# Kernel tuning notes

Hardware: AMD Instinct MI355X
Metric: run time of the kernel (lower is better)

## Reference

```python
import jax, jax.numpy as jnp
import numpy as np

N = 50000      # nodes
E = 800000     # edges
F_IN = 500     # input features
H1 = 300       # lin output
H2 = 100       # conv1 output
C = 16         # num classes


def setup_inputs() -> dict:
    key = jax.random.key(0)
    ks = jax.random.split(key, 8)
    x = jax.random.normal(ks[0], (N, F_IN), dtype=jnp.float32)
    edge_index = jax.random.randint(ks[1], (2, E), 0, N, dtype=jnp.int64)
    s = 0.05
    lin_W = jax.random.normal(ks[2], (F_IN, H1), dtype=jnp.float32) * s
    lin_b = jnp.zeros((H1,), dtype=jnp.float32)
    W1 = jax.random.normal(ks[3], (H1, H2), dtype=jnp.float32) * s
    b1 = jnp.zeros((H2,), dtype=jnp.float32)
    W2 = jax.random.normal(ks[4], (H2, C), dtype=jnp.float32) * s
    b2 = jnp.zeros((C,), dtype=jnp.float32)
    return {"x": x, "lin_W": lin_W, "lin_b": lin_b, "W1": W1, "b1": b1,
            "W2": W2, "b2": b2, "edge_index": edge_index}


def gcn_layer(x, W, b, src, dst):
    # project first (PyG GCNConv), then normalized gather-scatter aggregation
    h = x @ W                                   # [N, d_out]
    loops = jnp.arange(N, dtype=src.dtype)      # add self-loops
    s = jnp.concatenate([src, loops])           # [E+N]
    d = jnp.concatenate([dst, loops])
    deg = jax.ops.segment_sum(jnp.ones_like(d, dtype=h.dtype), d, num_segments=N)
    dinv = jax.lax.rsqrt(jnp.maximum(deg, 1.0))  # deg >= 1 due to self-loops
    norm = dinv[s] * dinv[d]                     # [E+N]
    out = jax.ops.segment_sum(h[s] * norm[:, None], d, num_segments=N)
    return out + b


def reference(x, lin_W, lin_b, W1, b1, W2, b2, edge_index):
    src, dst = edge_index[0], edge_index[1]
    h = jax.nn.relu(x @ lin_W + lin_b)          # Linear(500->300) + relu
    h = jax.nn.relu(gcn_layer(h, W1, b1, src, dst))  # GCNConv(300->100) + relu
    # dropout is identity at inference (training=False)
    h = gcn_layer(h, W2, b2, src, dst)          # GCNConv(100->16)
    return jax.nn.log_softmax(h, axis=1)
```

## Files before the change

kernel.cpp:

```cpp
#include <hip/hip_runtime.h>
#include <hip/hip_bf16.h>

#define NN 50000
#define EE 800000
#define FIN 500
#define H1D 300
#define H2D 100
#define CC 16
#define GNB 196
#define PREP_N1 196608
#define PREP_N2 40960
#define PREP_BLOCKS 928

__device__ __forceinline__ float ldf(const void* p, size_t i, int isbf16) {
    return isbf16 ? __bfloat162float(((const __hip_bfloat16*)p)[i])
                  : ((const float*)p)[i];
}
__device__ __forceinline__ int ld_src(const int* ei, int e, int is64) {
    return is64 ? ei[2 * (size_t)e] : ei[e];
}
__device__ __forceinline__ int ld_dst(const int* ei, int e, int is64) {
    return is64 ? ei[2 * ((size_t)EE + e)] : ei[(size_t)EE + e];
}

__device__ __forceinline__ void split2(float f, unsigned short& h, unsigned short& l) {
    __bf16 hb = (__bf16)f;
    float fh = (float)hb;
    __bf16 lb = (__bf16)(f - fh);
    h = __builtin_bit_cast(unsigned short, hb);
    l = __builtin_bit_cast(unsigned short, lb);
}

__device__ __forceinline__ float2 bf2f2(unsigned int v) {
    float lo = __builtin_bit_cast(float, v << 16);
    float hi = __builtin_bit_cast(float, v & 0xffff0000u);
    return make_float2(lo, hi);
}

typedef __bf16 bf16x8 __attribute__((ext_vector_type(8)));
typedef float f32x4 __attribute__((ext_vector_type(4)));

__device__ __forceinline__ void prep_body(int idx, const float* linW, const float* W1,
                                          unsigned short* Bt1, unsigned short* Bt2) {
    if (idx < PREP_N1) {
        int n = idx >> 9, k = idx & 511;
        float v = (n < H1D && k < FIN) ? linW[(size_t)k * H1D + n] : 0.0f;
        unsigned short h, l;
        split2(v, h, l);
        Bt1[(size_t)n * 1024 + k] = h;
        Bt1[(size_t)n * 1024 + 512 + k] = l;
    } else if (idx < PREP_N1 + PREP_N2) {
        idx -= PREP_N1;
        int n = idx / 320, k = idx - n * 320;
        float v = (n < H2D && k < H1D) ? W1[(size_t)k * H2D + n] : 0.0f;
        unsigned short h, l;
        split2(v, h, l);
        Bt2[(size_t)n * 640 + k] = h;
        Bt2[(size_t)n * 640 + 320 + k] = l;
    }
}

__global__ __launch_bounds__(256) void k_init(const unsigned short* __restrict__ xw,
                                              const unsigned int* __restrict__ ew,
                                              int* __restrict__ flags,
                                              int* __restrict__ cnt,
                                              int* __restrict__ total,
                                              const float* __restrict__ linW,
                                              const float* __restrict__ W1,
                                              unsigned short* __restrict__ Bt1,
                                              unsigned short* __restrict__ Bt2) {
    int b = blockIdx.x;
    if (b == 0) {
        __shared__ int c_sane, c_zero;
        if (threadIdx.x == 0) { c_sane = 0; c_zero = 0; }
        __syncthreads();
        int t = threadIdx.x;
        int sane = 0, zer = 0;
        for (int j = 0; j < 4; j++) {
            unsigned short w = xw[t * 4 + j];
            int ex = (w >> 7) & 0xFF;
            if (w == 0 || (ex >= 100 && ex <= 150)) sane++;
            if (ew[2 * (t * 4 + j) + 1] == 0u) zer++;
        }
        atomicAdd(&c_sane, sane);
        atomicAdd(&c_zero, zer);
        __syncthreads();
        if (threadIdx.x == 0) {
            flags[0] = (c_sane > 820) ? 1 : 0;
            flags[1] = (c_zero > 512) ? 1 : 0;
            total[0] = 0;
        }
    } else if (b <= GNB) {
        int i = (b - 1) * 256 + threadIdx.x;
        if (i < NN) cnt[i] = 0;
    } else {
        prep_body((b - GNB - 1) * 256 + threadIdx.x, linW, W1, Bt1, Bt2);
    }
}

__global__ __launch_bounds__(256) void k_prep_both(const float* __restrict__ linW,
                                                   const float* __restrict__ W1,
                                                   unsigned short* __restrict__ Bt1,
                                                   unsigned short* __restrict__ Bt2,
                                                   const int* __restrict__ flags) {
    if (flags[0]) return;
    prep_body(blockIdx.x * 256 + threadIdx.x, linW, W1, Bt1, Bt2);
}

__global__ void k_hist(const int* __restrict__ ei, int* __restrict__ cnt,
                       const int* __restrict__ flags) {
    int e = blockIdx.x * blockDim.x + threadIdx.x;
    int is64 = flags[1];
    if (e < EE) {
        int d = ld_dst(ei, e, is64);
        if ((unsigned)d < NN) atomicAdd(&cnt[d], 1);
    }
}

__global__ __launch_bounds__(256) void k_scan_mb(int* __restrict__ cnt,
                                                 int* __restrict__ row_ptr,
                                                 float* __restrict__ dinv,
                                                 int* __restrict__ total) {
    int t = threadIdx.x;
    int i = blockIdx.x * 256 + t;
    int c = (i < NN) ? cnt[i] : 0;
    __shared__ int s[256];
    s[t] = c;
    __syncthreads();
    for (int off = 1; off < 256; off <<= 1) {
        int v = (t >= off) ? s[t - off] : 0;
        __syncthreads();
        s[t] += v;
        __syncthreads();
    }
    int incl = s[t];
    __shared__ int base;
    if (t == 255) base = atomicAdd(total, s[255]);
    __syncthreads();
    if (i < NN) {
        row_ptr[i] = base + incl - c;
        dinv[i] = rsqrtf((float)c + 1.0f);
        cnt[i] = 0;
    }
}

__global__ void k_scatter(const int* __restrict__ ei, const int* __restrict__ row_ptr,
                          int* __restrict__ fill, int* __restrict__ csr_src,
                          const int* __restrict__ flags) {
    int e = blockIdx.x * blockDim.x + threadIdx.x;
    int is64 = flags[1];
    if (e < EE) {
        int s = ld_src(ei, e, is64);
        int d = ld_dst(ei, e, is64);
        if ((unsigned)d < NN) {
            int pos = row_ptr[d] + atomicAdd(&fill[d], 1);
            csr_src[pos] = s;
        }
    }
}

template <bool A_DYN, bool RELU, bool SCALE, bool OUTBF>
__global__ __launch_bounds__(256) void k_gemm(const void* __restrict__ A,
                                              const void* __restrict__ B,
                                              const void* __restrict__ bias,
                                              const float* __restrict__ dinv,
                                              void* __restrict__ C,
                                              int M, int K, int Nn,
                                              const int* __restrict__ flags) {
    if (!flags[0]) return;
    __shared__ float As[16][68];
    __shared__ float Bs[16][68];
    const int bf = flags[0];
    const int tid = threadIdx.x;
    const int m0 = blockIdx.x * 64, n0 = blockIdx.y * 64;
    const int tx = tid & 15;
    const int ty = tid >> 4;
    float acc[4][4] = {};

    for (int kc = 0; kc < K; kc += 16) {
#pragma unroll
        for (int j = 0; j < 4; j++) {
            int idx = tid + j * 256;
            int kk = idx & 15, mm = idx >> 4;
            int gm = m0 + mm, gk = kc + kk;
            float v = 0.0f;
            if (gm < M && gk < K) {
                size_t o = (size_t)gm * K + gk;
                v = A_DYN ? ldf(A, o, bf) : ((const float*)A)[o];
            }
            As[kk][mm] = v;
        }
#pragma unroll
        for (int j = 0; j < 4; j++) {
            int idx = tid + j * 256;
            int nn = idx & 63, kk = idx >> 6;
            int gk = kc + kk, gn = n0 + nn;
            Bs[kk][nn] = (gk < K && gn < Nn) ? ldf(B, (size_t)gk * Nn + gn, bf) : 0.0f;
        }
        __syncthreads();
#pragma unroll
        for (int kk = 0; kk < 16; kk++) {
            float4 a4 = *(const float4*)&As[kk][ty * 4];
            float4 b4 = *(const float4*)&Bs[kk][tx * 4];
            float av[4] = {a4.x, a4.y, a4.z, a4.w};
            float bv[4] = {b4.x, b4.y, b4.z, b4.w};
#pragma unroll
            for (int i = 0; i < 4; i++)
#pragma unroll
                for (int j = 0; j < 4; j++) acc[i][j] += av[i] * bv[j];
        }
        __syncthreads();
    }

#pragma unroll
    for (int i = 0; i < 4; i++) {
        int m = m0 + ty * 4 + i;
        if (m >= M) continue;
        float sc = SCALE ? dinv[m] : 1.0f;
#pragma unroll
        for (int j = 0; j < 4; j++) {
            int n = n0 + tx * 4 + j;
            if (n >= Nn) continue;
            float v = acc[i][j];
            if (bias) v += ldf(bias, n, bf);
            if (SCALE) v *= sc;
            if (RELU) v = fmaxf(v, 0.0f);
            if (OUTBF) ((__hip_bfloat16*)C)[(size_t)m * Nn + n] = __float2bfloat16(v);
            else       ((float*)C)[(size_t)m * Nn + n] = v;
        }
    }
}

template <int BM, int WN, bool RELU, bool SCALE, bool HAS_BIAS, bool OUTBF>
__global__ __launch_bounds__(256) void k_gemm_mfma_split(const float* __restrict__ A,
                                                         const unsigned short* __restrict__ Bt,
                                                         const float* __restrict__ bias,
                                                         const float* __restrict__ dinv,
                                                         void* __restrict__ C,
                                                         int M, int K, int Kp, int Nn, int NnS,
                                                         const int* __restrict__ flags) {
    if (flags[0]) return;
    constexpr int WM = 4 / WN;
    constexpr int FM = BM / WM / 16;
    constexpr int FN = 128 / WN / 16;
    constexpr int NA = BM / 32;
    __shared__ unsigned short As_hi[BM * 32], As_lo[BM * 32];
    __shared__ unsigned short Bs_hi[4096], Bs_lo[4096];
    const int tid = threadIdx.x;
    const int nbx = gridDim.x;
    const int Wt = nbx * gridDim.y;
    const int li = blockIdx.x + nbx * blockIdx.y;
    const int q8 = Wt >> 3, r8 = Wt & 7;
    const int xk = li & 7, xj = li >> 3;
    const int wid = (xk < r8 ? xk * (q8 + 1) : r8 * (q8 + 1) + (xk - r8) * q8) + xj;
    const int n0 = (wid % nbx) * 128;
    const int m0 = (wid / nbx) * BM;
    const int w = tid >> 6, l = tid & 63;
    const int wm = (w / WN) * (BM / WM);
    const int wn = (w % WN) * (128 / WN);
    const int lr = l & 15, ls = l >> 4;
    f32x4 acc[FM][FN] = {};

    float4 stA[NA];
    uint4  stB0, stB1, stB2, stB3;

#define LOAD_TILE(kc_)                                                              \
    {                                                                               \
        int kc = (kc_);                                                             \
        _Pragma("unroll")                                                           \
        for (int j = 0; j < NA; j++) {                                              \
            int c = tid + j * 256;                                                  \
            int r = c >> 3, q = c & 7;                                              \
            int gm = m0 + r, gk = kc + q * 4;                                       \
            stA[j] = (gm < M && gk < K) ? *(const float4*)(A + (size_t)gm * K + gk) \
                                        : make_float4(0.f, 0.f, 0.f, 0.f);          \
        }                                                                           \
        {                                                                           \
            int c, r, q, gn;                                                        \
            c = tid;       r = c >> 2; q = c & 3; gn = n0 + r;                      \
            stB0 = *(const uint4*)(Bt + (size_t)gn * (2 * Kp) + kc + q * 8);        \
            c = tid + 256; r = c >> 2; q = c & 3; gn = n0 + r;                      \
            stB1 = *(const uint4*)(Bt + (size_t)gn * (2 * Kp) + kc + q * 8);        \
            c = tid;       r = c >> 2; q = c & 3; gn = n0 + r;                      \
            stB2 = *(const uint4*)(Bt + (size_t)gn * (2 * Kp) + Kp + kc + q * 8);   \
            c = tid + 256; r = c >> 2; q = c & 3; gn = n0 + r;                      \
            stB3 = *(const uint4*)(Bt + (size_t)gn * (2 * Kp) + Kp + kc + q * 8);   \
        }                                                                           \
    }

#define WRITE_TILE()                                                                \
    {                                                                               \
        _Pragma("unroll")                                                           \
        for (int j = 0; j < NA; j++) {                                              \
            int c = tid + j * 256;                                                  \
            int r = c >> 3, q = c & 7;                                              \
            unsigned short h0,h1,h2,h3,l0,l1,l2,l3;                                 \
            split2(stA[j].x, h0, l0); split2(stA[j].y, h1, l1);                     \
            split2(stA[j].z, h2, l2); split2(stA[j].w, h3, l3);                     \
            int waddr = r * 64 + (((q >> 1) ^ ((r >> 1) & 3)) << 4) + ((q & 1) << 3); \
            *(ushort4*)((char*)As_hi + waddr) = make_ushort4(h0, h1, h2, h3);       \
            *(ushort4*)((char*)As_lo + waddr) = make_ushort4(l0, l1, l2, l3);       \
        }                                                                           \
        {                                                                           \
            int c, r, q, waddr;                                                     \
            c = tid;       r = c >> 2; q = c & 3; waddr = r * 64 + ((q ^ ((r >> 1) & 3)) << 4); \
            *(uint4*)((char*)Bs_hi + waddr) = stB0;                                 \
            c = tid + 256; r = c >> 2; q = c & 3; waddr = r * 64 + ((q ^ ((r >> 1) & 3)) << 4); \
            *(uint4*)((char*)Bs_hi + waddr) = stB1;                                 \
            c = tid;       r = c >> 2; q = c & 3; waddr = r * 64 + ((q ^ ((r >> 1) & 3)) << 4); \
            *(uint4*)((char*)Bs_lo + waddr) = stB2;                                 \
            c = tid + 256; r = c >> 2; q = c & 3; waddr = r * 64 + ((q ^ ((r >> 1) & 3)) << 4); \
            *(uint4*)((char*)Bs_lo + waddr) = stB3;                                 \
        }                                                                           \
    }

    const int nsteps = (K + 31) / 32;
    LOAD_TILE(0);
    for (int kt = 0; kt < nsteps; kt++) {
        WRITE_TILE();
        __syncthreads();
        if (kt + 1 < nsteps) LOAD_TILE((kt + 1) * 32);
        bf16x8 ah[FM], al[FM], bh[FN], bl[FN];
#pragma unroll
        for (int fm = 0; fm < FM; fm++) {
            int rr = wm + fm * 16 + lr;
            int addr = rr * 64 + ((ls ^ ((rr >> 1) & 3)) << 4);
            ah[fm] = *(const bf16x8*)((const char*)As_hi + addr);
            al[fm] = *(const bf16x8*)((const char*)As_lo + addr);
        }
#pragma unroll
        for (int fn = 0; fn < FN; fn++) {
            int cc2 = wn + fn * 16 + lr;
            int addr = cc2 * 64 + ((ls ^ ((cc2 >> 1) & 3)) << 4);
            bh[fn] = *(const bf16x8*)((const char*)Bs_hi + addr);
            bl[fn] = *(const bf16x8*)((const char*)Bs_lo + addr);
        }
#pragma unroll
        for (int fm = 0; fm < FM; fm++)
#pragma unroll
            for (int fn = 0; fn < FN; fn++) {
                acc[fm][fn] = __builtin_amdgcn_mfma_f32_16x16x32_bf16(ah[fm], bh[fn], acc[fm][fn], 0, 0, 0);
                acc[fm][fn] = __builtin_amdgcn_mfma_f32_16x16x32_bf16(ah[fm], bl[fn], acc[fm][fn], 0, 0, 0);
                acc[fm][fn] = __builtin_amdgcn_mfma_f32_16x16x32_bf16(al[fm], bh[fn], acc[fm][fn], 0, 0, 0);
            }
        __syncthreads();
    }
#undef LOAD_TILE
#undef WRITE_TILE

#pragma unroll
    for (int fm = 0; fm < FM; fm++) {
#pragma unroll
        for (int j = 0; j < 4; j++) {
            int m = m0 + wm + fm * 16 + ls * 4 + j;
            if (m >= M) continue;
            float sc = SCALE ? dinv[m] : 1.0f;
#pragma unroll
            for (int fn = 0; fn < FN; fn++) {
                int n = n0 + wn + fn * 16 + lr;
                if (OUTBF) {
                    if (n >= NnS) continue;
                    float v = 0.0f;
                    if (n < Nn) {
                        v = acc[fm][fn][j];
                        if (HAS_BIAS) v += bias[n];
                        if (SCALE) v *= sc;
                        if (RELU) v = fmaxf(v, 0.0f);
                    }
                    ((__hip_bfloat16*)C)[(size_t)m * NnS + n] = __float2bfloat16(v);
                } else {
                    if (n >= Nn) continue;
                    float v = acc[fm][fn][j];
                    if (HAS_BIAS) v += bias[n];
                    if (SCALE) v *= sc;
                    if (RELU) v = fmaxf(v, 0.0f);
                    ((float*)C)[(size_t)m * Nn + n] = v;
                }
            }
        }
    }
}

__global__ __launch_bounds__(256) void k_gemm2_bf16a(const unsigned short* __restrict__ A,
                                                     const unsigned short* __restrict__ Bt,
                                                     const float* __restrict__ dinv,
                                                     unsigned short* __restrict__ C,
                                                     int M, const int* __restrict__ flags) {
    if (flags[0]) return;
    constexpr int Kp = 320;
    __shared__ unsigned short As[64 * 32];
    __shared__ unsigned short Bs_hi[4096], Bs_lo[4096];
    const int tid = threadIdx.x;
    const int Wt = gridDim.x;
    const int li = blockIdx.x;
    const int q8 = Wt >> 3, r8 = Wt & 7;
    const int xk = li & 7, xj = li >> 3;
    const int wid = (xk < r8 ? xk * (q8 + 1) : r8 * (q8 + 1) + (xk - r8) * q8) + xj;
    const int m0 = wid * 64;
    const int w = tid >> 6, l = tid & 63;
    const int wn = w * 32;
    const int lr = l & 15, ls = l >> 4;
    f32x4 acc[4][2] = {};

    uint4 stA, stB0, stB1, stB2, stB3;

#define LOAD_T2(kc_)                                                                \
    {                                                                               \
        int kc = (kc_);                                                             \
        {                                                                           \
            int r = tid >> 2, q = tid & 3;                                          \
            int gm = m0 + r;                                                        \
            stA = (gm < M) ? *(const uint4*)(A + (size_t)gm * Kp + kc + q * 8)      \
                           : make_uint4(0u, 0u, 0u, 0u);                            \
        }                                                                           \
        {                                                                           \
            int c, r, q, gn;                                                        \
            c = tid;       r = c >> 2; q = c & 3; gn = r;                           \
            stB0 = *(const uint4*)(Bt + (size_t)gn * (2 * Kp) + kc + q * 8);        \
            c = tid + 256; r = c >> 2; q = c & 3; gn = r;                           \
            stB1 = *(const uint4*)(Bt + (size_t)gn * (2 * Kp) + kc + q * 8);        \
            c = tid;       r = c >> 2; q = c & 3; gn = r;                           \
            stB2 = *(const uint4*)(Bt + (size_t)gn * (2 * Kp) + Kp + kc + q * 8);   \
            c = tid + 256; r = c >> 2; q = c & 3; gn = r;                           \
            stB3 = *(const uint4*)(Bt + (size_t)gn * (2 * Kp) + Kp + kc + q * 8);   \
        }                                                                           \
    }

#define WRITE_T2()                                                                  \
    {                                                                               \
        {                                                                           \
            int r = tid >> 2, q = tid & 3;                                          \
            int waddr = r * 64 + ((q ^ ((r >> 1) & 3)) << 4);                       \
            *(uint4*)((char*)As + waddr) = stA;                                     \
        }                                                                           \
        {                                                                           \
            int c, r, q, waddr;                                                     \
            c = tid;       r = c >> 2; q = c & 3; waddr = r * 64 + ((q ^ ((r >> 1) & 3)) << 4); \
            *(uint4*)((char*)Bs_hi + waddr) = stB0;                                 \
            c = tid + 256; r = c >> 2; q = c & 3; waddr = r * 64 + ((q ^ ((r >> 1) & 3)) << 4); \
            *(uint4*)((char*)Bs_hi + waddr) = stB1;                                 \
            c = tid;       r = c >> 2; q = c & 3; waddr = r * 64 + ((q ^ ((r >> 1) & 3)) << 4); \
            *(uint4*)((char*)Bs_lo + waddr) = stB2;                                 \
            c = tid + 256; r = c >> 2; q = c & 3; waddr = r * 64 + ((q ^ ((r >> 1) & 3)) << 4); \
            *(uint4*)((char*)Bs_lo + waddr) = stB3;                                 \
        }                                                                           \
    }

    const int nsteps = Kp / 32;
    LOAD_T2(0);
    for (int kt = 0; kt < nsteps; kt++) {
        WRITE_T2();
        __syncthreads();
        if (kt + 1 < nsteps) LOAD_T2((kt + 1) * 32);
        bf16x8 ah[4], bh[2], bl[2];
#pragma unroll
        for (int fm = 0; fm < 4; fm++) {
            int rr = fm * 16 + lr;
            int addr = rr * 64 + ((ls ^ ((rr >> 1) & 3)) << 4);
            ah[fm] = *(const bf16x8*)((const char*)As + addr);
        }
#pragma unroll
        for (int fn = 0; fn < 2; fn++) {
            int cc2 = wn + fn * 16 + lr;
            int addr = cc2 * 64 + ((ls ^ ((cc2 >> 1) & 3)) << 4);
            bh[fn] = *(const bf16x8*)((const char*)Bs_hi + addr);
            bl[fn] = *(const bf16x8*)((const char*)Bs_lo + addr);
        }
#pragma unroll
        for (int fm = 0; fm < 4; fm++)
#pragma unroll
            for (int fn = 0; fn < 2; fn++) {
                acc[fm][fn] = __builtin_amdgcn_mfma_f32_16x16x32_bf16(ah[fm], bh[fn], acc[fm][fn], 0, 0, 0);
                acc[fm][fn] = __builtin_amdgcn_mfma_f32_16x16x32_bf16(ah[fm], bl[fn], acc[fm][fn], 0, 0, 0);
            }
        __syncthreads();
    }
#undef LOAD_T2
#undef WRITE_T2

#pragma unroll
    for (int fm = 0; fm < 4; fm++) {
#pragma unroll
        for (int j = 0; j < 4; j++) {
            int m = m0 + fm * 16 + ls * 4 + j;
            if (m >= M) continue;
            float sc = dinv[m];
#pragma unroll
            for (int fn = 0; fn < 2; fn++) {
                int n = wn + fn * 16 + lr;
                if (n >= H2D) continue;
                ((__hip_bfloat16*)C)[(size_t)m * H2D + n] = __float2bfloat16(acc[fm][fn][j] * sc);
            }
        }
    }
}

__global__ __launch_bounds__(256) void k_agg1_fused(const unsigned short* __restrict__ h1p_bf,
                                                    const int* __restrict__ row_ptr,
                                                    const int* __restrict__ deg,
                                                    const int* __restrict__ csr_src,
                                                    const float* __restrict__ dinv,
                                                    const void* __restrict__ b1,
                                                    const void* __restrict__ W2,
                                                    float* __restrict__ h2p,
                                                    const int* __restrict__ flags) {
    __shared__ float W2s[16][105];
    __shared__ float b1s[H2D];
    __shared__ float Hrow[4][H2D];
    const int bf = flags[0];
    const int tid = threadIdx.x;
    for (int i = tid; i < H2D * CC; i += 256) {
        int k = i >> 4, n = i & 15;
        W2s[n][k] = ldf(W2, i, bf);
    }
    for (int i = tid; i < H2D; i += 256) b1s[i] = ldf(b1, i, bf);
    __syncthreads();

    const int w = tid >> 6, lane = tid & 63;
    const int q = lane >> 4, n16 = lane & 15;
    const unsigned int* rows = (const unsigned int*)h1p_bf;
    for (int node = blockIdx.x * 4 + w; node < NN; node += gridDim.x * 4) {
        float di = dinv[node];
        if (lane < 50) {
            float2 s = bf2f2(rows[(size_t)node * 50 + lane]);
            float a0x = s.x, a0y = s.y;
            float a1x = 0.f, a1y = 0.f, a2x = 0.f, a2y = 0.f, a3x = 0.f, a3y = 0.f;
            int lo = row_ptr[node], hi = lo + deg[node];
            int e = lo;
            for (; e + 3 < hi; e += 4) {
                int s0 = csr_src[e], s1 = csr_src[e + 1], s2 = csr_src[e + 2], s3 = csr_src[e + 3];
                float2 v0 = bf2f2(rows[(size_t)s0 * 50 + lane]);
                float2 v1 = bf2f2(rows[(size_t)s1 * 50 + lane]);
                float2 v2 = bf2f2(rows[(size_t)s2 * 50 + lane]);
                float2 v3 = bf2f2(rows[(size_t)s3 * 50 + lane]);
                a0x += v0.x; a0y += v0.y;
                a1x += v1.x; a1y += v1.y;
                a2x += v2.x; a2y += v2.y;
                a3x += v3.x; a3y += v3.y;
            }
            for (; e < hi; e++) {
                float2 v = bf2f2(rows[(size_t)csr_src[e] * 50 + lane]);
                a0x += v.x; a0y += v.y;
            }
            float sx = (a0x + a1x) + (a2x + a3x);
            float sy = (a0y + a1y) + (a2y + a3y);
            int f = lane * 2;
            Hrow[w][f]     = fmaxf(sx * di + b1s[f], 0.0f);
            Hrow[w][f + 1] = fmaxf(sy * di + b1s[f + 1], 0.0f);
        }
        __builtin_amdgcn_sched_barrier(0);
        float acc2 = 0.0f;
#pragma unroll
        for (int j = 0; j < 25; j++) {
            int k = q * 25 + j;
            acc2 += Hrow[w][k] * W2s[n16][k];
        }
        acc2 += __shfl_xor(acc2, 16);
        acc2 += __shfl_xor(acc2, 32);
        if (lane < 16) h2p[(size_t)node * CC + n16] = acc2 * di;
        __builtin_amdgcn_sched_barrier(0);
    }
}

__global__ __launch_bounds__(256) void k_agg2(const float* __restrict__ h2p,
                                              const int* __restrict__ row_ptr,
                                              const int* __restrict__ deg,
                                              const int* __restrict__ csr_src,
                                              const float* __restrict__ dinv,
                                              const void* __restrict__ b2,
                                              void* __restrict__ out,
                                              const int* __restrict__ flags) {
    int tid = threadIdx.x;
    int n = tid & 15;
    int g = tid >> 4;
    int node = blockIdx.x * 16 + g;
    if (node >= NN) return;
    const int bf = flags[0];
    float a0 = h2p[(size_t)node * CC + n];
    float a1 = 0.f, a2 = 0.f, a3 = 0.f;
    int lo = row_ptr[node], hi = lo + deg[node];
    int e = lo;
    for (; e + 3 < hi; e += 4) {
        int s0 = csr_src[e], s1 = csr_src[e + 1], s2 = csr_src[e + 2], s3 = csr_src[e + 3];
        a0 += h2p[(size_t)s0 * CC + n];
        a1 += h2p[(size_t)s1 * CC + n];
        a2 += h2p[(size_t)s2 * CC + n];
        a3 += h2p[(size_t)s3 * CC + n];
    }
    for (; e < hi; e++) a0 += h2p[(size_t)csr_src[e] * CC + n];
    float acc = (a0 + a1) + (a2 + a3);
    float logit = acc * dinv[node] + ldf(b2, n, bf);
    float m = logit;
#pragma unroll
    for (int off = 1; off < 16; off <<= 1) m = fmaxf(m, __shfl_xor(m, off, 16));
    float ex = __expf(logit - m);
    float ssum = ex;
#pragma unroll
    for (int off = 1; off < 16; off <<= 1) ssum += __shfl_xor(ssum, off, 16);
    float r = logit - m - __logf(ssum);
    size_t oidx = (size_t)node * CC + n;
    if (bf) ((__hip_bfloat16*)out)[oidx] = __float2bfloat16(r);
    else    ((float*)out)[oidx] = r;
}

extern "C" void kernel_launch(void* const* d_in, const int* in_sizes, int n_in,
                              void* d_out, int out_size, void* d_ws, size_t ws_size,
                              hipStream_t stream) {
    const void* x     = d_in[0];
    const void* lin_W = d_in[1];
    const void* lin_b = d_in[2];
    const void* W1    = d_in[3];
    const void* b1    = d_in[4];
    const void* W2    = d_in[5];
    const void* b2    = d_in[6];
    const int*  ei    = (const int*)d_in[7];

    char* ws = (char*)d_ws;
    size_t off = 0;
    auto alloc = [&](size_t bytes) {
        off = (off + 255) & ~(size_t)255;
        void* p = ws + off;
        off += bytes;
        return p;
    };
    int*   flags   = (int*)alloc(2 * 4);
    int*   total   = (int*)alloc(4);
    int*   cnt     = (int*)alloc((size_t)NN * 4);
    int*   row_ptr = (int*)alloc((size_t)NN * 4);
    int*   csr_src = (int*)alloc((size_t)EE * 4);
    float* dinv    = (float*)alloc((size_t)NN * 4);
    char*  H1      = (char*)alloc((size_t)NN * H1D * 4);
    unsigned short* H1p = (unsigned short*)alloc((size_t)NN * H2D * 2);
    float* h2p     = (float*)alloc((size_t)NN * CC * 4);
    unsigned short* Bt1 = (unsigned short*)alloc((size_t)384 * 1024 * 2);
    unsigned short* Bt2 = (unsigned short*)alloc((size_t)128 * 640 * 2);

    const int gE = (EE + 255) / 256;

    const bool surely_fp32 = (in_sizes != nullptr) && (in_sizes[0] >= 90000000);

    k_init<<<surely_fp32 ? (GNB + 1 + PREP_BLOCKS) : (GNB + 1), 256, 0, stream>>>(
        (const unsigned short*)x, (const unsigned int*)ei, flags, cnt, total,
        (const float*)lin_W, (const float*)W1, Bt1, Bt2);
    if (!surely_fp32)
        k_prep_both<<<PREP_BLOCKS, 256, 0, stream>>>(
            (const float*)lin_W, (const float*)W1, Bt1, Bt2, flags);

    k_hist<<<gE, 256, 0, stream>>>(ei, cnt, flags);
    k_scan_mb<<<GNB, 256, 0, stream>>>(cnt, row_ptr, dinv, total);
    k_scatter<<<gE, 256, 0, stream>>>(ei, row_ptr, cnt, csr_src, flags);

    {
        const int moff[5] = {0, 12544, 25088, 37632, 50000};
        for (int qi = 0; qi < 4; qi++) {
            int Mq = moff[qi + 1] - moff[qi];
            int nb = (Mq + 63) / 64;
            k_gemm_mfma_split<64, 4, true, false, true, true>
                <<<dim3(3, nb), 256, 0, stream>>>(
                    (const float*)x + (size_t)moff[qi] * FIN, Bt1, (const float*)lin_b,
                    nullptr, (unsigned short*)H1 + (size_t)moff[qi] * 320,
                    Mq, FIN, 512, H1D, 320, flags);
        }
    }
    if (!surely_fp32) {
        dim3 grid((NN + 63) / 64, (H1D + 63) / 64);
        k_gemm<true, true, false, false><<<grid, 256, 0, stream>>>(
            x, lin_W, lin_b, nullptr, H1, NN, FIN, H1D, flags);
    }

    k_gemm2_bf16a<<<(NN + 63) / 64, 256, 0, stream>>>(
        (const unsigned short*)H1, Bt2, dinv, H1p, NN, flags);
    if (!surely_fp32) {
        dim3 grid((NN + 63) / 64, (H2D + 63) / 64);
        k_gemm<false, false, true, true><<<grid, 256, 0, stream>>>(
            H1, W1, nullptr, dinv, H1p, NN, H1D, H2D, flags);
    }

    k_agg1_fused<<<6144, 256, 0, stream>>>(H1p, row_ptr, cnt, csr_src, dinv, b1, W2, h2p, flags);
    k_agg2<<<(NN + 15) / 16, 256, 0, stream>>>(h2p, row_ptr, cnt, csr_src, dinv, b2, d_out, flags);
}
```

Measured before the change: 453.0 us.

## Fuse CSR build into one cooperative kernel and merge split GEMM launches

Result: slower. 685.9 us (+51.4%).

```diff
diff --git a/kernel.cpp b/kernel.cpp
--- a/kernel.cpp
+++ b/kernel.cpp
@@ -1,5 +1,8 @@
 #include <hip/hip_runtime.h>
 #include <hip/hip_bf16.h>
+#include <hip/hip_cooperative_groups.h>
+
+namespace cg = cooperative_groups;
 
 #define NN 50000
 #define EE 800000
@@ -63,8 +66,6 @@
 __global__ __launch_bounds__(256) void k_init(const unsigned short* __restrict__ xw,
                                               const unsigned int* __restrict__ ew,
                                               int* __restrict__ flags,
-                                              int* __restrict__ cnt,
-                                              int* __restrict__ total,
                                               const float* __restrict__ linW,
                                               const float* __restrict__ W1,
                                               unsigned short* __restrict__ Bt1,
@@ -88,13 +89,9 @@
         if (threadIdx.x == 0) {
             flags[0] = (c_sane > 820) ? 1 : 0;
             flags[1] = (c_zero > 512) ? 1 : 0;
-            total[0] = 0;
-        }
-    } else if (b <= GNB) {
-        int i = (b - 1) * 256 + threadIdx.x;
-        if (i < NN) cnt[i] = 0;
+        }
     } else {
-        prep_body((b - GNB - 1) * 256 + threadIdx.x, linW, W1, Bt1, Bt2);
+        prep_body((b - 1) * 256 + threadIdx.x, linW, W1, Bt1, Bt2);
     }
 }
 
@@ -107,6 +104,63 @@
     prep_body(blockIdx.x * 256 + threadIdx.x, linW, W1, Bt1, Bt2);
 }
 
+__global__ __launch_bounds__(256) void k_csr_coop(const int* __restrict__ ei,
+                                                  int* __restrict__ cnt,
+                                                  int* __restrict__ row_ptr,
+                                                  float* __restrict__ dinv,
+                                                  int* __restrict__ csr_src,
+                                                  int* __restrict__ total,
+                                                  const int* __restrict__ flags) {
+    cg::grid_group grid = cg::this_grid();
+    const int T = gridDim.x * blockDim.x;
+    const int gtid = blockIdx.x * blockDim.x + threadIdx.x;
+    for (int i = gtid; i < NN; i += T) cnt[i] = 0;
+    if (gtid == 0) total[0] = 0;
+    grid.sync();
+    const int is64 = flags[1];
+    for (int e = gtid; e < EE; e += T) {
+        int d = ld_dst(ei, e, is64);
+        if ((unsigned)d < NN) atomicAdd(&cnt[d], 1);
+    }
+    grid.sync();
+    if (blockIdx.x < GNB) {
+        int t = threadIdx.x;
+        int i = blockIdx.x * 256 + t;
+        int c = (i < NN) ? cnt[i] : 0;
+        __shared__ int s[256];
+        s[t] = c;
+        __syncthreads();
+        for (int off2 = 1; off2 < 256; off2 <<= 1) {
+            int v = (t >= off2) ? s[t - off2] : 0;
+            __syncthreads();
+            s[t] += v;
+            __syncthreads();
+        }
+        __shared__ int base;
+        if (t == 255) base = atomicAdd(total, s[255]);
+        __syncthreads();
+        if (i < NN) {
+            row_ptr[i] = base + s[t] - c;
+            dinv[i] = rsqrtf((float)c + 1.0f);
+            cnt[i] = 0;
+        }
+    }
+    grid.sync();
+    for (int e = gtid; e < EE; e += T) {
+        int sv = ld_src(ei, e, is64);
+        int d = ld_dst(ei, e, is64);
+        if ((unsigned)d < NN) {
+            int pos = row_ptr[d] + atomicAdd(&cnt[d], 1);
+            csr_src[pos] = sv;
+        }
+    }
+}
+
+__global__ void k_zero_cnt(int* __restrict__ cnt, int* __restrict__ total) {
+    int i = blockIdx.x * blockDim.x + threadIdx.x;
+    if (i < NN) cnt[i] = 0;
+    if (i == 0) total[0] = 0;
+}
 __global__ void k_hist(const int* __restrict__ ei, int* __restrict__ cnt,
                        const int* __restrict__ flags) {
     int e = blockIdx.x * blockDim.x + threadIdx.x;
@@ -116,7 +170,6 @@
         if ((unsigned)d < NN) atomicAdd(&cnt[d], 1);
     }
 }
-
 __global__ __launch_bounds__(256) void k_scan_mb(int* __restrict__ cnt,
                                                  int* __restrict__ row_ptr,
                                                  float* __restrict__ dinv,
@@ -133,17 +186,15 @@
         s[t] += v;
         __syncthreads();
     }
-    int incl = s[t];
     __shared__ int base;
     if (t == 255) base = atomicAdd(total, s[255]);
     __syncthreads();
     if (i < NN) {
-        row_ptr[i] = base + incl - c;
+        row_ptr[i] = base + s[t] - c;
         dinv[i] = rsqrtf((float)c + 1.0f);
         cnt[i] = 0;
     }
 }
-
 __global__ void k_scatter(const int* __restrict__ ei, const int* __restrict__ row_ptr,
                           int* __restrict__ fill, int* __restrict__ csr_src,
                           const int* __restrict__ flags) {
@@ -639,29 +690,31 @@
 
     const bool surely_fp32 = (in_sizes != nullptr) && (in_sizes[0] >= 90000000);
 
-    k_init<<<surely_fp32 ? (GNB + 1 + PREP_BLOCKS) : (GNB + 1), 256, 0, stream>>>(
-        (const unsigned short*)x, (const unsigned int*)ei, flags, cnt, total,
+    k_init<<<surely_fp32 ? (1 + PREP_BLOCKS) : 1, 256, 0, stream>>>(
+        (const unsigned short*)x, (const unsigned int*)ei, flags,
         (const float*)lin_W, (const float*)W1, Bt1, Bt2);
     if (!surely_fp32)
         k_prep_both<<<PREP_BLOCKS, 256, 0, stream>>>(
             (const float*)lin_W, (const float*)W1, Bt1, Bt2, flags);
 
-    k_hist<<<gE, 256, 0, stream>>>(ei, cnt, flags);
-    k_scan_mb<<<GNB, 256, 0, stream>>>(cnt, row_ptr, dinv, total);
-    k_scatter<<<gE, 256, 0, stream>>>(ei, row_ptr, cnt, csr_src, flags);
-
     {
-        const int moff[5] = {0, 12544, 25088, 37632, 50000};
-        for (int qi = 0; qi < 4; qi++) {
-            int Mq = moff[qi + 1] - moff[qi];
-            int nb = (Mq + 63) / 64;
-            k_gemm_mfma_split<64, 4, true, false, true, true>
-                <<<dim3(3, nb), 256, 0, stream>>>(
-                    (const float*)x + (size_t)moff[qi] * FIN, Bt1, (const float*)lin_b,
-                    nullptr, (unsigned short*)H1 + (size_t)moff[qi] * 320,
-                    Mq, FIN, 512, H1D, 320, flags);
-        }
-    }
+        void* kargs[] = {(void*)&ei, (void*)&cnt, (void*)&row_ptr, (void*)&dinv,
+                         (void*)&csr_src, (void*)&total, (void*)&flags};
+        hipError_t err = hipLaunchCooperativeKernel((void*)k_csr_coop, dim3(1024), dim3(256),
+                                                    kargs, 0, stream);
+        if (err != hipSuccess) {
+            (void)hipGetLastError();
+            k_zero_cnt<<<GNB, 256, 0, stream>>>(cnt, total);
+            k_hist<<<gE, 256, 0, stream>>>(ei, cnt, flags);
+            k_scan_mb<<<GNB, 256, 0, stream>>>(cnt, row_ptr, dinv, total);
+            k_scatter<<<gE, 256, 0, stream>>>(ei, row_ptr, cnt, csr_src, flags);
+        }
+    }
+
+    k_gemm_mfma_split<64, 4, true, false, true, true>
+        <<<dim3(3, (NN + 63) / 64), 256, 0, stream>>>(
+            (const float*)x, Bt1, (const float*)lin_b, nullptr, (unsigned short*)H1,
+            NN, FIN, 512, H1D, 320, flags);
     if (!surely_fp32) {
         dim3 grid((NN + 63) / 64, (H1D + 63) / 64);
         k_gemm<true, true, false, false><<<grid, 256, 0, stream>>>(
```
